# Kernel tuning notes

Hardware: AMD Instinct MI355X
Metric: run time of the kernel (lower is better)

Reference implementation:

```python
import jax, jax.numpy as jnp
import numpy as np

NX, T_IN, T_OUT = 256, 16, 128
STATE, PSIZE = 1, 4
WIDTH, DEPTH = 128, 4
BATCH = 4


def _build_edges(B):
    # Faithful vectorized replica of create_graph_structure (incl. the
    # batch-mixing .view(2,-1) on a (B,2,E) tensor).
    ng = NX * T_OUT
    # spatial edges: loops t outer, i inner, fwd/bwd interleaved
    a = (np.arange(T_OUT)[:, None] * NX + np.arange(NX - 1)[None, :]).reshape(-1)
    sp = np.stack([np.stack([a, a + 1], 1), np.stack([a + 1, a], 1)], 1).reshape(-1, 2)
    # temporal edges: loops x outer, t inner, fwd/bwd interleaved
    b = (np.arange(NX)[:, None] + np.arange(T_OUT - 1)[None, :] * NX).reshape(-1)
    tp = np.stack([np.stack([b, b + NX], 1), np.stack([b + NX, b], 1)], 1).reshape(-1, 2)
    base = np.concatenate([sp, tp], 0).T  # (2, E)
    ei = base[None, :, :] + (np.arange(B) * ng)[:, None, None]  # (B, 2, E)
    return ei.reshape(2, -1)  # row-major flatten, same as torch .view(2, -1)


def _layernorm(x, g, b, eps=1e-5):
    mu = x.mean(-1, keepdims=True)
    var = x.var(-1, keepdims=True)  # biased, same as torch LayerNorm
    return (x - mu) * jax.lax.rsqrt(var + eps) * g + b


def setup_inputs():
    key = jax.random.key(0)
    ks = jax.random.split(key, 8)
    d_in = STATE + PSIZE + 2
    return {
        "u0": jax.random.normal(ks[0], (BATCH, NX, T_IN, STATE), jnp.float32),
        "P": jax.random.normal(ks[1], (BATCH, PSIZE), jnp.float32),
        "W_in": jax.random.normal(ks[2], (d_in, WIDTH), jnp.float32) / np.sqrt(d_in),
        "b_in": jnp.zeros((WIDTH,), jnp.float32),
        "Wg": jax.random.normal(ks[3], (DEPTH, WIDTH, WIDTH), jnp.float32) / np.sqrt(WIDTH),
        "bg": jnp.zeros((DEPTH, WIDTH), jnp.float32),
        "gamma": jnp.ones((DEPTH, WIDTH), jnp.float32),
        "beta": jnp.zeros((DEPTH, WIDTH), jnp.float32),
        "W_out": jax.random.normal(ks[4], (WIDTH, STATE), jnp.float32) / np.sqrt(WIDTH),
        "b_out": jnp.zeros((STATE,), jnp.float32),
    }


def reference(u0, P, W_in, b_in, Wg, bg, gamma, beta, W_out, b_out):
    B = u0.shape[0]
    ng = NX * T_OUT
    N = B * ng

    ei = _build_edges(B)
    loops = np.arange(N)
    src = jnp.asarray(np.concatenate([ei[0], loops]))  # GCN adds self-loops
    dst = jnp.asarray(np.concatenate([ei[1], loops]))
    deg = jnp.zeros((N,), jnp.float32).at[dst].add(1.0)  # in-degree incl. self-loop
    dis = jnp.where(deg > 0, jax.lax.rsqrt(deg), 0.0)
    norm = (dis[src] * dis[dst])[:, None]  # symmetric GCN normalization

    # grid features flattened x-major (matches meshgrid 'ij' reshape(-1,1))
    xg = jnp.repeat(jnp.linspace(0.0, 1.0, NX), T_OUT)[None, :, None]
    tg = jnp.tile(jnp.linspace(0.0, 1.0, T_OUT), NX)[None, :, None]

    # bilinear resize (nx_in, T_in) -> (NX, T_OUT), align_corners=False semantics
    u0i = jax.image.resize(u0, (B, NX, T_OUT, STATE), "bilinear").reshape(B, ng, STATE)
    Pex = jnp.broadcast_to(P[:, None, :], (B, ng, PSIZE))
    feat = jnp.concatenate(
        [u0i, Pex, jnp.broadcast_to(xg, (B, ng, 1)), jnp.broadcast_to(tg, (B, ng, 1))], -1
    )
    x = (feat @ W_in + b_in).reshape(N, WIDTH)

    for l in range(DEPTH):
        h = x @ Wg[l]                      # GCNConv linear
        msg = h[src] * norm                # gather + normalize
        h = jax.ops.segment_sum(msg, dst, num_segments=N) + bg[l]  # scatter-add
        h = _layernorm(h, gamma[l], beta[l])
        x = jax.nn.relu(h + x)             # residual then ReLU

    out = x @ W_out + b_out
    return out.reshape(B, NX, T_OUT, STATE)
```

## Files before the change

kernel.cpp:

```cpp
#include <hip/hip_runtime.h>
#include <hip/hip_bf16.h>

#define NXX 256
#define NG 32768
#define WID 128

typedef short bf16x8 __attribute__((ext_vector_type(8)));
typedef float f32x4 __attribute__((ext_vector_type(4)));
typedef unsigned int u32x4 __attribute__((ext_vector_type(4)));

__device__ __forceinline__ unsigned short rne_bf16(float x) {
    unsigned int u = __float_as_uint(x);
    return (unsigned short)((u + 0x7fffu + ((u >> 16) & 1u)) >> 16);
}

__global__ __launch_bounds__(64) void prep_kernel(
    const float* __restrict__ Wg, unsigned short* __restrict__ Bfrag) {
    const int e  = blockIdx.x;
    const int lv = threadIdx.x;
    const int l  = e >> 5;
    const int kc = (e >> 3) & 3;
    const int nt = e & 7;
    const int n  = nt * 16 + (lv & 15);
    const int g  = lv >> 4;
#pragma unroll
    for (int j = 0; j < 8; ++j) {
        const int ch = kc * 32 + ((j >> 2) << 4) + (g << 2) + (j & 3);
        float v = Wg[(size_t)l * 16384 + (size_t)ch * WID + n];
        Bfrag[(size_t)e * 512 + lv * 8 + j] = rne_bf16(v);
    }
}

__device__ __forceinline__ unsigned int pack_bf2(float a, float b) {
    union { __hip_bfloat162 h2; unsigned int u; } cv;
    cv.h2 = __float22bfloat162_rn(make_float2(a, b));
    return cv.u;
}

union fragu { bf16x8 f; u32x4 u; };

#define GLOAD_LDS16(gsrc, ldst)                                              \
    __builtin_amdgcn_global_load_lds(                                        \
        (const __attribute__((address_space(1))) void*)(gsrc),               \
        (__attribute__((address_space(3))) void*)(ldst), 16, 0, 0)

__global__ __launch_bounds__(256) void fused_kernel(
    const float* __restrict__ u0, const float* __restrict__ P,
    const float* __restrict__ W_in, const float* __restrict__ b_in,
    const unsigned short* __restrict__ Bfrag,
    const float* __restrict__ bg, const float* __restrict__ gamma,
    const float* __restrict__ beta, const float* __restrict__ W_out,
    const float* __restrict__ b_out, float* __restrict__ out)
{
    __shared__ __align__(16) char Wlds[32768];

    const int tid  = threadIdx.x;
    const int w    = tid >> 6;
    const int lane = tid & 63;
    const int l15  = lane & 15;
    const int lhi  = lane >> 4;

    const int blk  = blockIdx.x;
    const int b    = blk >> 9;
    const int ublk = (blk & 511) << 6;

    const int u  = ublk + 16 * w + l15;
    const int ix = u >> 7;
    const int t  = u & 127;

    const char* gB = (const char*)Bfrag;

#pragma unroll
    for (int i = 0; i < 8; ++i) {
        const int chunk = w * 8 + i;
        GLOAD_LDS16(gB + chunk * 1024 + lane * 16, Wlds + chunk * 1024);
    }

    float c1, c2;
    {
        int gi = u & 255, gt = u >> 8;
        int d  = (gi > 0) + (gi < 255) + (gt > 0) + (gt < 127);
        float deg = 2.f * (float)d + 1.f;
        c1 = 2.f * (float)d * rsqrtf(deg);
        c2 = 1.f / deg;
    }

    float featA[7], featB[7];
    {
        float s  = ((float)t + 0.5f) * 0.125f - 0.5f;
        float fs = floorf(s);
        int   t0 = (int)fs;
        float wt = s - fs;
        int t0c = t0 < 0 ? 0 : (t0 > 15 ? 15 : t0);
        int t1n = t0 + 1;
        int t1c = t1n < 0 ? 0 : (t1n > 15 ? 15 : t1n);
        const float* urA = u0 + ((size_t)b * NXX + ix) * 16;
        const float* urB = u0 + ((size_t)(b + 2) * NXX + ix) * 16;
        featA[0] = urA[t0c] * (1.f - wt) + urA[t1c] * wt;
        featB[0] = urB[t0c] * (1.f - wt) + urB[t1c] * wt;
#pragma unroll
        for (int f = 0; f < 4; ++f) {
            featA[1 + f] = P[b * 4 + f];
            featB[1 + f] = P[(b + 2) * 4 + f];
        }
        featA[5] = featB[5] = (float)ix * (1.f / 255.f);
        featA[6] = featB[6] = (float)t  * (1.f / 127.f);
    }

    float xr0[8][4], xr1[8][4];
#pragma unroll
    for (int nt = 0; nt < 8; ++nt) {
        const int c = nt * 16 + 4 * lhi;
        float4 bi4 = *(const float4*)(b_in + c);
        float4 wf[7];
#pragma unroll
        for (int f = 0; f < 7; ++f) wf[f] = *(const float4*)(W_in + f * WID + c);
#pragma unroll
        for (int r = 0; r < 4; ++r) {
            float a0 = ((const float*)&bi4)[r];
            float a1 = a0;
#pragma unroll
            for (int f = 0; f < 7; ++f) {
                float wv = ((const float*)&wf[f])[r];
                a0 = fmaf(featA[f], wv, a0);
                a1 = fmaf(featB[f], wv, a1);
            }
            xr0[nt][r] = a0;
            xr1[nt][r] = a1;
        }
    }

    __syncthreads();

    const char* wl = Wlds + lane * 16;

    for (int l = 0; l < 4; ++l) {
        f32x4 acc0[8], acc1[8];
#pragma unroll
        for (int nt = 0; nt < 8; ++nt) {
            acc0[nt] = (f32x4){0.f, 0.f, 0.f, 0.f};
            acc1[nt] = (f32x4){0.f, 0.f, 0.f, 0.f};
        }
#pragma unroll
        for (int kc = 0; kc < 4; ++kc) {
            fragu x0f, x1f;
            x0f.u = (u32x4){pack_bf2(xr0[2 * kc][0],     xr0[2 * kc][1]),
                            pack_bf2(xr0[2 * kc][2],     xr0[2 * kc][3]),
                            pack_bf2(xr0[2 * kc + 1][0], xr0[2 * kc + 1][1]),
                            pack_bf2(xr0[2 * kc + 1][2], xr0[2 * kc + 1][3])};
            x1f.u = (u32x4){pack_bf2(xr1[2 * kc][0],     xr1[2 * kc][1]),
                            pack_bf2(xr1[2 * kc][2],     xr1[2 * kc][3]),
                            pack_bf2(xr1[2 * kc + 1][0], xr1[2 * kc + 1][1]),
                            pack_bf2(xr1[2 * kc + 1][2], xr1[2 * kc + 1][3])};
#pragma unroll
            for (int nt = 0; nt < 8; ++nt) {
                bf16x8 bh = *(const bf16x8*)(wl + (kc * 8 + nt) * 1024);
                acc0[nt] = __builtin_amdgcn_mfma_f32_16x16x32_bf16(bh, x0f.f, acc0[nt], 0, 0, 0);
                acc1[nt] = __builtin_amdgcn_mfma_f32_16x16x32_bf16(bh, x1f.f, acc1[nt], 0, 0, 0);
            }
        }

        if (l < 3) {
            __syncthreads();
#pragma unroll
            for (int i = 0; i < 8; ++i) {
                const int chunk = w * 8 + i;
                GLOAD_LDS16(gB + (l + 1) * 32768 + chunk * 1024 + lane * 16,
                            Wlds + chunk * 1024);
            }
        }

        float s0 = 0.f, q0 = 0.f, s1 = 0.f, q1 = 0.f;
#pragma unroll
        for (int nt = 0; nt < 8; ++nt) {
            float4 bg4 = *(const float4*)(bg + l * WID + nt * 16 + 4 * lhi);
#pragma unroll
            for (int r = 0; r < 4; ++r) {
                float bgr = ((const float*)&bg4)[r];
                float h0 = acc0[nt][r];
                float h1 = acc1[nt][r];
                float a0 = h0 + bgr;
                float a1 = fmaf(c1, h0, fmaf(c2, h1, bgr));
                acc0[nt][r] = a0;
                acc1[nt][r] = a1;
                s0 += a0;  q0 = fmaf(a0, a0, q0);
                s1 += a1;  q1 = fmaf(a1, a1, q1);
            }
        }
        s0 += __shfl_xor(s0, 16);  q0 += __shfl_xor(q0, 16);
        s1 += __shfl_xor(s1, 16);  q1 += __shfl_xor(q1, 16);
        s0 += __shfl_xor(s0, 32);  q0 += __shfl_xor(q0, 32);
        s1 += __shfl_xor(s1, 32);  q1 += __shfl_xor(q1, 32);
        float mu0 = s0 * (1.f / 128.f);
        float mu1 = s1 * (1.f / 128.f);
        float rs0 = rsqrtf(q0 * (1.f / 128.f) - mu0 * mu0 + 1e-5f);
        float rs1 = rsqrtf(q1 * (1.f / 128.f) - mu1 * mu1 + 1e-5f);
#pragma unroll
        for (int nt = 0; nt < 8; ++nt) {
            const int c = nt * 16 + 4 * lhi;
            float4 g4 = *(const float4*)(gamma + l * WID + c);
            float4 e4 = *(const float4*)(beta  + l * WID + c);
#pragma unroll
            for (int r = 0; r < 4; ++r) {
                float gv = ((const float*)&g4)[r];
                float ev = ((const float*)&e4)[r];
                float n0 = fmaf((acc0[nt][r] - mu0) * rs0, gv, ev);
                float n1 = fmaf((acc1[nt][r] - mu1) * rs1, gv, ev);
                xr0[nt][r] = fmaxf(n0 + xr0[nt][r], 0.f);
                xr1[nt][r] = fmaxf(n1 + xr1[nt][r], 0.f);
            }
        }

        if (l < 3) __syncthreads();
    }

    float p0 = 0.f, p1 = 0.f;
#pragma unroll
    for (int nt = 0; nt < 8; ++nt) {
        float4 wo4 = *(const float4*)(W_out + nt * 16 + 4 * lhi);
#pragma unroll
        for (int r = 0; r < 4; ++r) {
            float wv = ((const float*)&wo4)[r];
            p0 = fmaf(xr0[nt][r], wv, p0);
            p1 = fmaf(xr1[nt][r], wv, p1);
        }
    }
    p0 += __shfl_xor(p0, 16);  p1 += __shfl_xor(p1, 16);
    p0 += __shfl_xor(p0, 32);  p1 += __shfl_xor(p1, 32);
    if (lhi == 0) {
        float bo = b_out[0];
        out[(size_t)b * NG + u]       = p0 + bo;
        out[(size_t)(b + 2) * NG + u] = p1 + bo;
    }
}

extern "C" void kernel_launch(void* const* d_in, const int* in_sizes, int n_in,
                              void* d_out, int out_size, void* d_ws, size_t ws_size,
                              hipStream_t stream) {
    const float* u0    = (const float*)d_in[0];
    const float* P     = (const float*)d_in[1];
    const float* W_in  = (const float*)d_in[2];
    const float* b_in  = (const float*)d_in[3];
    const float* Wg    = (const float*)d_in[4];
    const float* bg    = (const float*)d_in[5];
    const float* gamma = (const float*)d_in[6];
    const float* beta  = (const float*)d_in[7];
    const float* W_out = (const float*)d_in[8];
    const float* b_out = (const float*)d_in[9];

    unsigned short* Bfrag = (unsigned short*)d_ws;

    prep_kernel<<<128, 64, 0, stream>>>(Wg, Bfrag);
    fused_kernel<<<1024, 256, 0, stream>>>(
        u0, P, W_in, b_in, Bfrag, bg, gamma, beta, W_out, b_out, (float*)d_out);
}
```

Before: 66.73 us.

## Double-buffer layer weights in LDS and stage LayerNorm params in shared memory

Blocks grow to 512 threads covering twice as many nodes, and each block now keeps two 32KB LDS weight buffers. The next layer's weights are prefetched into the spare buffer while the current layer's MFMAs run, replacing the barrier-then-reload between layers. The bg/gamma/beta vectors are copied into LDS once rather than read from global memory every layer. The cost is 70KB of LDS per block, which limits residency, and the code still relies on __syncthreads between layers for the prefetch to be visible.

```diff
diff --git a/kernel.cpp b/kernel.cpp
--- a/kernel.cpp
+++ b/kernel.cpp
@@ -44,7 +44,7 @@
         (const __attribute__((address_space(1))) void*)(gsrc),               \
         (__attribute__((address_space(3))) void*)(ldst), 16, 0, 0)
 
-__global__ __launch_bounds__(256) void fused_kernel(
+__global__ __launch_bounds__(512, 4) void fused_kernel(
     const float* __restrict__ u0, const float* __restrict__ P,
     const float* __restrict__ W_in, const float* __restrict__ b_in,
     const unsigned short* __restrict__ Bfrag,
@@ -52,7 +52,12 @@
     const float* __restrict__ beta, const float* __restrict__ W_out,
     const float* __restrict__ b_out, float* __restrict__ out)
 {
-    __shared__ __align__(16) char Wlds[32768];
+    __shared__ __align__(16) char SMEM[2 * 32768 + 3 * 2048];
+    char*  Wbuf0 = SMEM;
+    char*  Wbuf1 = SMEM + 32768;
+    float* Pbg   = (float*)(SMEM + 65536);
+    float* Pgm   = (float*)(SMEM + 65536 + 2048);
+    float* Pbe   = (float*)(SMEM + 65536 + 4096);
 
     const int tid  = threadIdx.x;
     const int w    = tid >> 6;
@@ -61,8 +66,8 @@
     const int lhi  = lane >> 4;
 
     const int blk  = blockIdx.x;
-    const int b    = blk >> 9;
-    const int ublk = (blk & 511) << 6;
+    const int b    = blk >> 8;
+    const int ublk = (blk & 255) << 7;
 
     const int u  = ublk + 16 * w + l15;
     const int ix = u >> 7;
@@ -71,9 +76,15 @@
     const char* gB = (const char*)Bfrag;
 
 #pragma unroll
-    for (int i = 0; i < 8; ++i) {
-        const int chunk = w * 8 + i;
-        GLOAD_LDS16(gB + chunk * 1024 + lane * 16, Wlds + chunk * 1024);
+    for (int i = 0; i < 4; ++i) {
+        const int chunk = w * 4 + i;
+        GLOAD_LDS16(gB + chunk * 1024 + lane * 16, Wbuf0 + chunk * 1024);
+    }
+    {
+        const int sel = w >> 1, half = (w & 1) * 1024;
+        if (sel == 0) GLOAD_LDS16((const char*)bg    + half + lane * 16, (char*)Pbg + half);
+        else if (sel == 1) GLOAD_LDS16((const char*)gamma + half + lane * 16, (char*)Pgm + half);
+        else if (sel == 2) GLOAD_LDS16((const char*)beta  + half + lane * 16, (char*)Pbe + half);
     }
 
     float c1, c2;
@@ -132,9 +143,19 @@
 
     __syncthreads();
 
-    const char* wl = Wlds + lane * 16;
-
     for (int l = 0; l < 4; ++l) {
+        const char* wl = ((l & 1) ? Wbuf1 : Wbuf0) + lane * 16;
+
+        if (l < 3) {
+            char* nb = ((l & 1) ? Wbuf0 : Wbuf1);
+            const char* gsrc = gB + (l + 1) * 32768;
+#pragma unroll
+            for (int i = 0; i < 4; ++i) {
+                const int chunk = w * 4 + i;
+                GLOAD_LDS16(gsrc + chunk * 1024 + lane * 16, nb + chunk * 1024);
+            }
+        }
+
         f32x4 acc0[8], acc1[8];
 #pragma unroll
         for (int nt = 0; nt < 8; ++nt) {
@@ -160,20 +181,10 @@
             }
         }
 
-        if (l < 3) {
-            __syncthreads();
-#pragma unroll
-            for (int i = 0; i < 8; ++i) {
-                const int chunk = w * 8 + i;
-                GLOAD_LDS16(gB + (l + 1) * 32768 + chunk * 1024 + lane * 16,
-                            Wlds + chunk * 1024);
-            }
-        }
-
         float s0 = 0.f, q0 = 0.f, s1 = 0.f, q1 = 0.f;
 #pragma unroll
         for (int nt = 0; nt < 8; ++nt) {
-            float4 bg4 = *(const float4*)(bg + l * WID + nt * 16 + 4 * lhi);
+            float4 bg4 = *(const float4*)(Pbg + l * WID + nt * 16 + 4 * lhi);
 #pragma unroll
             for (int r = 0; r < 4; ++r) {
                 float bgr = ((const float*)&bg4)[r];
@@ -198,8 +209,8 @@
 #pragma unroll
         for (int nt = 0; nt < 8; ++nt) {
             const int c = nt * 16 + 4 * lhi;
-            float4 g4 = *(const float4*)(gamma + l * WID + c);
-            float4 e4 = *(const float4*)(beta  + l * WID + c);
+            float4 g4 = *(const float4*)(Pgm + l * WID + c);
+            float4 e4 = *(const float4*)(Pbe + l * WID + c);
 #pragma unroll
             for (int r = 0; r < 4; ++r) {
                 float gv = ((const float*)&g4)[r];
@@ -251,6 +262,6 @@
     unsigned short* Bfrag = (unsigned short*)d_ws;
 
     prep_kernel<<<128, 64, 0, stream>>>(Wg, Bfrag);
-    fused_kernel<<<1024, 256, 0, stream>>>(
+    fused_kernel<<<512, 512, 0, stream>>>(
         u0, P, W_in, b_in, Bfrag, bg, gamma, beta, W_out, b_out, (float*)d_out);
 }
```

Result: slower. 135.3 us (+102.7%).
